# Performance work log

Measured on AMD Instinct MI355X. Metric: run time of the kernel, lower is better.

## Reference

```python
import jax, jax.numpy as jnp
import numpy as np
from jax import lax

EPS = 1e-5
KS = 3
PAD = 1
C = 256
G = 8          # ska_groups
VG = 8         # verifier groups
B, H, W = 8, 128, 128


def _bn(y, gamma, beta, mean, var):
    # inference-mode BatchNorm2d
    inv = gamma / jnp.sqrt(var + EPS)
    return y * inv[None, :, None, None] + (beta - mean * inv)[None, :, None, None]


def setup_inputs() -> dict:
    key = jax.random.key(0)
    ks = jax.random.split(key, 12)
    x = jax.random.normal(ks[0], (B, C, H, W), jnp.float32)
    dynamic_weight = jax.random.normal(ks[1], (B, G, KS * KS, H, W), jnp.float32)
    roi_mask = jax.random.uniform(ks[2], (B, 1, H, W), jnp.float32)
    # local_verifier params: Conv2d_BN(C,C,ks=3,pad=1,groups=8) -> ReLU -> Conv2d_BN(C,C,ks=1)
    w1 = jax.random.normal(ks[3], (C, C // VG, 3, 3), jnp.float32) * 0.05
    g1 = jnp.ones((C,), jnp.float32)
    b1 = jnp.zeros((C,), jnp.float32)
    m1 = jax.random.normal(ks[4], (C,), jnp.float32) * 0.1
    v1 = jax.random.uniform(ks[5], (C,), jnp.float32) + 0.5
    w2 = jax.random.normal(ks[6], (C, C, 1, 1), jnp.float32) * 0.05
    g2 = jnp.ones((C,), jnp.float32)
    b2 = jnp.zeros((C,), jnp.float32)
    m2 = jax.random.normal(ks[7], (C,), jnp.float32) * 0.1
    v2 = jax.random.uniform(ks[8], (C,), jnp.float32) + 0.5
    return dict(x=x, dynamic_weight=dynamic_weight, roi_mask=roi_mask,
                w1=w1, g1=g1, b1=b1, m1=m1, v1=v1,
                w2=w2, g2=g2, b2=b2, m2=m2, v2=v2)


def reference(x, dynamic_weight, roi_mask, w1, g1, b1, m1, v1, w2, g2, b2, m2, v2):
    Bx, Cx, Hx, Wx = x.shape
    gc = Cx // G  # group_channels
    # SKA: spatially-varying 3x3 aggregation. Boundary-dependent slicing in the
    # original is equivalent to zero-padding x by PAD.
    x_pad = jnp.pad(x, ((0, 0), (0, 0), (PAD, PAD), (PAD, PAD)))
    xg = x_pad.reshape(Bx, G, gc, Hx + 2 * PAD, Wx + 2 * PAD)
    ska = jnp.zeros((Bx, G, gc, Hx, Wx), x.dtype)
    for kh in range(KS):
        for kw in range(KS):
            ska = ska + xg[:, :, :, kh:kh + Hx, kw:kw + Wx] * \
                  dynamic_weight[:, :, None, kh * KS + kw]
    ska = ska.reshape(Bx, Cx, Hx, Wx)
    # local verifier: grouped 3x3 conv + BN + ReLU + 1x1 conv + BN
    y = ska * roi_mask
    y = lax.conv_general_dilated(y, w1, (1, 1), 'SAME',
                                 feature_group_count=VG,
                                 dimension_numbers=('NCHW', 'OIHW', 'NCHW'))
    y = jax.nn.relu(_bn(y, g1, b1, m1, v1))
    y = lax.conv_general_dilated(y, w2, (1, 1), 'VALID',
                                 dimension_numbers=('NCHW', 'OIHW', 'NCHW'))
    y = _bn(y, g2, b2, m2, v2)
    return ska + y
```

## Files before the change

### kernel.cpp

```cpp
#include <hip/hip_runtime.h>
#include <hip/hip_bf16.h>


#define HW 16384
#define EPS 1e-5f

typedef __bf16 bf16x8 __attribute__((ext_vector_type(8)));
typedef short short8 __attribute__((ext_vector_type(8)));
typedef short short4v __attribute__((ext_vector_type(4)));
typedef float floatx4 __attribute__((ext_vector_type(4)));

__device__ __forceinline__ unsigned short f2bf(float f) {
  unsigned u = __builtin_bit_cast(unsigned, f);
  unsigned r = u + 0x7FFFu + ((u >> 16) & 1u);
  return (unsigned short)(r >> 16);
}

__device__ __forceinline__ floatx4 mfma16(short8 a, short8 b, floatx4 c) {
  return __builtin_amdgcn_mfma_f32_16x16x32_bf16(
      __builtin_bit_cast(bf16x8, a), __builtin_bit_cast(bf16x8, b), c, 0, 0, 0);
}

__global__ __launch_bounds__(256) void prepack(const float* __restrict__ w1,
                                               const float* __restrict__ w2,
                                               unsigned short* __restrict__ w1b,
                                               unsigned short* __restrict__ w2b) {
  int o = blockIdx.x * 256 + threadIdx.x;
  if (o < 73728) {
    int ci  = o & 31;
    int co  = (o >> 5) & 31;
    int khw = (o >> 10) % 9;
    int g   = (o >> 10) / 9;
    w1b[o] = f2bf(w1[((g * 32 + co) * 32 + ci) * 9 + khw]);
  } else {
    int p = o - 73728;
    w2b[p] = f2bf(w2[p]);
  }
}

__global__ __launch_bounds__(256, 4) void ska_kernel(
    const float* __restrict__ x, const float* __restrict__ dw,
    const float* __restrict__ roi, float* __restrict__ out,
    unsigned short* __restrict__ y0b) {
  __shared__ float dwf[9][2][32];
  __shared__ float roib[2][32];
  __shared__ unsigned short tile[2 * 32 * 36];

  int phys = blockIdx.x;
  int blk  = (phys & 7) * 2048 + (phys >> 3);
  int wt = blk & 3;
  int hp = (blk >> 2) & 63;
  int g  = (blk >> 8) & 7;
  int b  = blk >> 11;
  int h0 = hp * 2;
  int tid = threadIdx.x;
  int ci = tid >> 3;
  int wq = tid & 7;
  int w0 = wt * 32 + wq * 4;
  int c  = g * 32 + ci;

  if (tid < 160) {
    if (tid < 144) {
      int k = tid >> 4, r = (tid >> 3) & 1, w4 = (tid & 7) * 4;
      *(floatx4*)&dwf[k][r][w4] = *(const floatx4*)
          &dw[((size_t)(b * 8 + g) * 9 + k) * HW + (h0 + r) * 128 + wt * 32 + w4];
    } else {
      int i = tid - 144, r = i >> 3, w4 = (i & 7) * 4;
      *(floatx4*)&roib[r][w4] = *(const floatx4*)
          &roi[(size_t)b * HW + (h0 + r) * 128 + wt * 32 + w4];
    }
  }

  float xr[4][6];
#pragma unroll
  for (int rr = 0; rr < 4; ++rr) {
    int hh = h0 - 1 + rr;
    if ((unsigned)hh < 128u) {
      const float* xp = &x[((size_t)(b * 256 + c)) * HW + hh * 128 + w0];
      floatx4 m = *(const floatx4*)xp;
      xr[rr][0] = (w0 > 0) ? xp[-1] : 0.f;
      xr[rr][1] = m[0];
      xr[rr][2] = m[1];
      xr[rr][3] = m[2];
      xr[rr][4] = m[3];
      xr[rr][5] = (w0 < 124) ? xp[4] : 0.f;
    } else {
#pragma unroll
      for (int i = 0; i < 6; ++i) xr[rr][i] = 0.f;
    }
  }

  __syncthreads();

  size_t base = ((size_t)(b * 256 + c)) * HW + h0 * 128 + w0;
#pragma unroll
  for (int r = 0; r < 2; ++r) {
    float s[4] = {0.f, 0.f, 0.f, 0.f};
#pragma unroll
    for (int kh = 0; kh < 3; ++kh)
#pragma unroll
      for (int kw = 0; kw < 3; ++kw) {
        floatx4 wk = *(const floatx4*)&dwf[kh * 3 + kw][r][wq * 4];
#pragma unroll
        for (int j = 0; j < 4; ++j) s[j] += xr[r + kh][kw + j] * wk[j];
      }
    *(floatx4*)&out[base + r * 128] = (floatx4){s[0], s[1], s[2], s[3]};
    floatx4 rv = *(const floatx4*)&roib[r][wq * 4];
#pragma unroll
    for (int j = 0; j < 4; ++j)
      tile[(r * 32 + wq * 4 + j) * 36 + ci] = f2bf(s[j] * rv[j]);
  }

  __syncthreads();

  unsigned short* dst =
      y0b + ((size_t)(b * 8 + g) * HW + h0 * 128 + wt * 32) * 32;
  int row = tid >> 7, rest = tid & 127;
  int w = rest >> 2, kk = rest & 3;
  *(short8*)&dst[(size_t)row * 128 * 32 + w * 32 + kk * 8] =
      *(const short8*)&tile[(row * 32 + w) * 36 + kk * 8];
}

__global__ __launch_bounds__(256) void conv1_mfma(
    const unsigned short* __restrict__ y0, const unsigned short* __restrict__ w1b,
    const float* __restrict__ g1, const float* __restrict__ b1,
    const float* __restrict__ m1, const float* __restrict__ v1,
    unsigned short* __restrict__ h1t) {
  __shared__ unsigned short xt[324 * 40];

  int blk  = blockIdx.x;
  int tile = blk & 63;
  int g    = (blk >> 6) & 7;
  int b    = blk >> 9;
  int h0   = (tile >> 3) * 16;
  int w0   = (tile & 7) * 16;
  int tid  = threadIdx.x;

  const unsigned short* xsrc = y0 + (size_t)(b * 8 + g) * HW * 32;
  short8 sv[6];
#pragma unroll
  for (int t = 0; t < 6; ++t) {
    int j = tid + t * 256;
    short8 v = (short8){0, 0, 0, 0, 0, 0, 0, 0};
    if (j < 1296) {
      int r = j >> 2, part = j & 3;
      int yy = r / 18, xx = r - yy * 18;
      int gh = h0 - 1 + yy, gw = w0 - 1 + xx;
      if ((unsigned)gh < 128u && (unsigned)gw < 128u)
        v = *(const short8*)&xsrc[(size_t)(gh * 128 + gw) * 32 + part * 8];
    }
    sv[t] = v;
  }
#pragma unroll
  for (int t = 0; t < 6; ++t) {
    int j = tid + t * 256;
    if (j < 1296) {
      int r = j >> 2, part = j & 3;
      *(short8*)&xt[r * 40 + part * 8] = sv[t];
    }
  }

  int wv = tid >> 6, lane = tid & 63, q = lane >> 4, n = lane & 15;

  short8 bf[9][2];
  const unsigned short* wgb = w1b + (size_t)g * 9 * 32 * 32;
#pragma unroll
  for (int khw = 0; khw < 9; ++khw) {
#pragma unroll
    for (int half = 0; half < 2; ++half)
      bf[khw][half] =
          *(const short8*)&wgb[(khw * 32 + half * 16 + n) * 32 + q * 8];
  }

  __syncthreads();

  floatx4 acc[4][2];
#pragma unroll
  for (int r = 0; r < 4; ++r)
#pragma unroll
    for (int half = 0; half < 2; ++half) acc[r][half] = (floatx4){0.f, 0.f, 0.f, 0.f};

#pragma unroll
  for (int r = 0; r < 4; ++r) {
    int row = wv * 4 + r;
#pragma unroll
    for (int khw = 0; khw < 9; ++khw) {
      int kh = khw / 3, kw = khw % 3;
      short8 a = *(const short8*)&xt[((row + kh) * 18 + kw + n) * 40 + q * 8];
      acc[r][0] = mfma16(a, bf[khw][0], acc[r][0]);
      acc[r][1] = mfma16(a, bf[khw][1], acc[r][1]);
    }
  }

  float inv[2], bias[2];
#pragma unroll
  for (int half = 0; half < 2; ++half) {
    int cc = g * 32 + half * 16 + n;
    inv[half]  = g1[cc] * rsqrtf(v1[cc] + EPS);
    bias[half] = b1[cc] - m1[cc] * inv[half];
  }

  __syncthreads();

#pragma unroll
  for (int r = 0; r < 4; ++r) {
    int pr = (wv * 4 + r) * 16;
#pragma unroll
    for (int half = 0; half < 2; ++half) {
      int co = half * 16 + n;
#pragma unroll
      for (int reg = 0; reg < 4; ++reg) {
        int px = pr + q * 4 + reg;
        float v = fmaxf(acc[r][half][reg] * inv[half] + bias[half], 0.f);
        xt[px * 40 + co] = f2bf(v);
      }
    }
  }

  __syncthreads();

  unsigned short* hb = h1t + (size_t)(b * 8 + g) * HW * 32;
  int ph = tid >> 4, pw = tid & 15;
  size_t gp = (size_t)((h0 + ph) * 128 + (w0 + pw)) * 32;
#pragma unroll
  for (int k = 0; k < 4; ++k)
    *(short8*)&hb[gp + k * 8] = *(const short8*)&xt[tid * 40 + k * 8];
}

__global__ __launch_bounds__(256) void conv2_mfma(
    const unsigned short* __restrict__ h1t, const unsigned short* __restrict__ w2b,
    const float* __restrict__ g2, const float* __restrict__ b2,
    const float* __restrict__ m2, const float* __restrict__ v2,
    float* __restrict__ out) {
  __shared__ unsigned short As[3][2048];

  int blk = blockIdx.x;
  int b   = blk >> 8;
  int px0 = (blk & 255) * 64;
  int tid = threadIdx.x;
  int wv = tid >> 6, lane = tid & 63, q = lane >> 4, n = lane & 15;

  const unsigned short* sb = h1t + ((size_t)b * 8 * HW + px0) * 32;

#define STAGE(S, BUF)                                                         \
  __builtin_amdgcn_global_load_lds(                                           \
      (const __attribute__((address_space(1))) unsigned int*)(sb +            \
          (size_t)(S) * HW * 32 + wv * 512 + lane * 8),                       \
      (__attribute__((address_space(3))) unsigned int*)&As[BUF][wv * 512],    \
      16, 0, 0)

  floatx4 acc[4][4];
#pragma unroll
  for (int mt = 0; mt < 4; ++mt)
#pragma unroll
    for (int nt = 0; nt < 4; ++nt) acc[mt][nt] = (floatx4){0.f, 0.f, 0.f, 0.f};

  STAGE(0, 0);
  STAGE(1, 1);
  asm volatile("s_waitcnt vmcnt(1)");
  __syncthreads();

#pragma unroll
  for (int s = 0; s < 8; ++s) {
    if (s < 6) STAGE(s + 2, (s + 2) % 3);
    short8 bb[4];
#pragma unroll
    for (int nt = 0; nt < 4; ++nt)
      bb[nt] =
          *(const short8*)&w2b[(wv * 64 + nt * 16 + n) * 256 + s * 32 + q * 8];
    const unsigned short* Ab = &As[s % 3][0];
#pragma unroll
    for (int mt = 0; mt < 4; ++mt) {
      short8 a = *(const short8*)&Ab[(mt * 16 + n) * 32 + q * 8];
#pragma unroll
      for (int nt = 0; nt < 4; ++nt) acc[mt][nt] = mfma16(a, bb[nt], acc[mt][nt]);
    }
    if (s < 6) asm volatile("s_waitcnt vmcnt(1)");
    else if (s == 6) asm volatile("s_waitcnt vmcnt(0)");
    if (s < 7) __syncthreads();
  }
#undef STAGE

#pragma unroll
  for (int nt = 0; nt < 4; ++nt) {
    int co = wv * 64 + nt * 16 + n;
    float inv  = g2[co] * rsqrtf(v2[co] + EPS);
    float bias = b2[co] - m2[co] * inv;
    float* ob = out + (size_t)(b * 256 + co) * HW;
#pragma unroll
    for (int mt = 0; mt < 4; ++mt) {
      int px = px0 + mt * 16 + q * 4;
      float4 sv = *(float4*)&ob[px];
      sv.x += acc[mt][nt][0] * inv + bias;
      sv.y += acc[mt][nt][1] * inv + bias;
      sv.z += acc[mt][nt][2] * inv + bias;
      sv.w += acc[mt][nt][3] * inv + bias;
      *(float4*)&ob[px] = sv;
    }
  }
}

extern "C" void kernel_launch(void* const* d_in, const int* in_sizes, int n_in,
                              void* d_out, int out_size, void* d_ws,
                              size_t ws_size, hipStream_t stream) {
  const float* x   = (const float*)d_in[0];
  const float* dw  = (const float*)d_in[1];
  const float* roi = (const float*)d_in[2];
  const float* w1  = (const float*)d_in[3];
  const float* g1  = (const float*)d_in[4];
  const float* b1  = (const float*)d_in[5];
  const float* m1  = (const float*)d_in[6];
  const float* v1  = (const float*)d_in[7];
  const float* w2  = (const float*)d_in[8];
  const float* g2  = (const float*)d_in[9];
  const float* b2  = (const float*)d_in[10];
  const float* m2  = (const float*)d_in[11];
  const float* v2  = (const float*)d_in[12];
  float* out = (float*)d_out;

  char* ws = (char*)d_ws;
  unsigned short* y0b = (unsigned short*)ws;
  unsigned short* h1t = (unsigned short*)(ws + 67108864);
  unsigned short* w1b = (unsigned short*)(ws + 134217728);
  unsigned short* w2b = (unsigned short*)(ws + 134365184);

  prepack<<<544, 256, 0, stream>>>(w1, w2, w1b, w2b);
  ska_kernel<<<16384, 256, 0, stream>>>(x, dw, roi, out, y0b);
  conv1_mfma<<<4096, 256, 0, stream>>>(y0b, w1b, g1, b1, m1, v1, h1t);
  conv2_mfma<<<2048, 256, 0, stream>>>(h1t, w2b, g2, b2, m2, v2, out);
}
```

Measured before the change: 459.8 us.

## Fold weight prepack into SKA kernel and process one row per block

Removes the separate prepack launch by appending extra blocks to the SKA kernel that convert w1/w2 to bf16. Each SKA block now handles a single output row instead of two, loading the dynamic weights and ROI mask straight into registers instead of staging them in shared memory. This doubles the grid size and re-reads the halo rows of x more often, in exchange for dropping one kernel launch and one barrier. The tile padding and store width change to match the single-row layout.

```diff
diff --git a/kernel.cpp b/kernel.cpp
--- a/kernel.cpp
+++ b/kernel.cpp
@@ -21,104 +21,91 @@
       __builtin_bit_cast(bf16x8, a), __builtin_bit_cast(bf16x8, b), c, 0, 0, 0);
 }
 
-__global__ __launch_bounds__(256) void prepack(const float* __restrict__ w1,
-                                               const float* __restrict__ w2,
-                                               unsigned short* __restrict__ w1b,
-                                               unsigned short* __restrict__ w2b) {
-  int o = blockIdx.x * 256 + threadIdx.x;
-  if (o < 73728) {
-    int ci  = o & 31;
-    int co  = (o >> 5) & 31;
-    int khw = (o >> 10) % 9;
-    int g   = (o >> 10) / 9;
-    w1b[o] = f2bf(w1[((g * 32 + co) * 32 + ci) * 9 + khw]);
-  } else {
-    int p = o - 73728;
-    w2b[p] = f2bf(w2[p]);
-  }
-}
-
 __global__ __launch_bounds__(256, 4) void ska_kernel(
     const float* __restrict__ x, const float* __restrict__ dw,
     const float* __restrict__ roi, float* __restrict__ out,
-    unsigned short* __restrict__ y0b) {
-  __shared__ float dwf[9][2][32];
-  __shared__ float roib[2][32];
-  __shared__ unsigned short tile[2 * 32 * 36];
+    unsigned short* __restrict__ y0b,
+    const float* __restrict__ w1, const float* __restrict__ w2,
+    unsigned short* __restrict__ w1b, unsigned short* __restrict__ w2b) {
+  __shared__ unsigned short tile[32 * 34];
 
   int phys = blockIdx.x;
-  int blk  = (phys & 7) * 2048 + (phys >> 3);
+  int tid  = threadIdx.x;
+
+  if (phys >= 32768) {
+    int o = (phys - 32768) * 256 + tid;
+    if (o < 73728) {
+      int ci  = o & 31;
+      int co  = (o >> 5) & 31;
+      int khw = (o >> 10) % 9;
+      int g   = (o >> 10) / 9;
+      w1b[o] = f2bf(w1[((g * 32 + co) * 32 + ci) * 9 + khw]);
+    } else {
+      int p = o - 73728;
+      w2b[p] = f2bf(w2[p]);
+    }
+    return;
+  }
+
+  int blk = (phys & 7) * 4096 + (phys >> 3);
   int wt = blk & 3;
-  int hp = (blk >> 2) & 63;
-  int g  = (blk >> 8) & 7;
-  int b  = blk >> 11;
-  int h0 = hp * 2;
-  int tid = threadIdx.x;
+  int h  = (blk >> 2) & 127;
+  int g  = (blk >> 9) & 7;
+  int b  = blk >> 12;
   int ci = tid >> 3;
   int wq = tid & 7;
   int w0 = wt * 32 + wq * 4;
   int c  = g * 32 + ci;
 
-  if (tid < 160) {
-    if (tid < 144) {
-      int k = tid >> 4, r = (tid >> 3) & 1, w4 = (tid & 7) * 4;
-      *(floatx4*)&dwf[k][r][w4] = *(const floatx4*)
-          &dw[((size_t)(b * 8 + g) * 9 + k) * HW + (h0 + r) * 128 + wt * 32 + w4];
+  const float* dwb = dw + ((size_t)(b * 8 + g) * 9) * HW + h * 128 + w0;
+  floatx4 wv[9];
+#pragma unroll
+  for (int k = 0; k < 9; ++k) wv[k] = *(const floatx4*)&dwb[k * HW];
+
+  floatx4 rv = *(const floatx4*)&roi[(size_t)b * HW + h * 128 + w0];
+
+  size_t base = ((size_t)(b * 256 + c)) * HW + h * 128 + w0;
+  float xr[3][6];
+#pragma unroll
+  for (int kh = 0; kh < 3; ++kh) {
+    int hh = h + kh - 1;
+    if ((unsigned)hh < 128u) {
+      const float* xp = &x[base + (kh - 1) * 128];
+      floatx4 m = *(const floatx4*)xp;
+      xr[kh][0] = (w0 > 0) ? xp[-1] : 0.f;
+      xr[kh][1] = m[0];
+      xr[kh][2] = m[1];
+      xr[kh][3] = m[2];
+      xr[kh][4] = m[3];
+      xr[kh][5] = (w0 < 124) ? xp[4] : 0.f;
     } else {
-      int i = tid - 144, r = i >> 3, w4 = (i & 7) * 4;
-      *(floatx4*)&roib[r][w4] = *(const floatx4*)
-          &roi[(size_t)b * HW + (h0 + r) * 128 + wt * 32 + w4];
-    }
-  }
-
-  float xr[4][6];
-#pragma unroll
-  for (int rr = 0; rr < 4; ++rr) {
-    int hh = h0 - 1 + rr;
-    if ((unsigned)hh < 128u) {
-      const float* xp = &x[((size_t)(b * 256 + c)) * HW + hh * 128 + w0];
-      floatx4 m = *(const floatx4*)xp;
-      xr[rr][0] = (w0 > 0) ? xp[-1] : 0.f;
-      xr[rr][1] = m[0];
-      xr[rr][2] = m[1];
-      xr[rr][3] = m[2];
-      xr[rr][4] = m[3];
-      xr[rr][5] = (w0 < 124) ? xp[4] : 0.f;
-    } else {
-#pragma unroll
-      for (int i = 0; i < 6; ++i) xr[rr][i] = 0.f;
-    }
-  }
-
-  __syncthreads();
-
-  size_t base = ((size_t)(b * 256 + c)) * HW + h0 * 128 + w0;
-#pragma unroll
-  for (int r = 0; r < 2; ++r) {
-    float s[4] = {0.f, 0.f, 0.f, 0.f};
-#pragma unroll
-    for (int kh = 0; kh < 3; ++kh)
-#pragma unroll
-      for (int kw = 0; kw < 3; ++kw) {
-        floatx4 wk = *(const floatx4*)&dwf[kh * 3 + kw][r][wq * 4];
-#pragma unroll
-        for (int j = 0; j < 4; ++j) s[j] += xr[r + kh][kw + j] * wk[j];
-      }
-    *(floatx4*)&out[base + r * 128] = (floatx4){s[0], s[1], s[2], s[3]};
-    floatx4 rv = *(const floatx4*)&roib[r][wq * 4];
-#pragma unroll
-    for (int j = 0; j < 4; ++j)
-      tile[(r * 32 + wq * 4 + j) * 36 + ci] = f2bf(s[j] * rv[j]);
-  }
+#pragma unroll
+      for (int i = 0; i < 6; ++i) xr[kh][i] = 0.f;
+    }
+  }
+
+  float s[4] = {0.f, 0.f, 0.f, 0.f};
+#pragma unroll
+  for (int kh = 0; kh < 3; ++kh)
+#pragma unroll
+    for (int kw = 0; kw < 3; ++kw) {
+      floatx4 wk = wv[kh * 3 + kw];
+#pragma unroll
+      for (int j = 0; j < 4; ++j) s[j] += xr[kh][kw + j] * wk[j];
+    }
+
+  *(floatx4*)&out[base] = (floatx4){s[0], s[1], s[2], s[3]};
+
+#pragma unroll
+  for (int j = 0; j < 4; ++j)
+    tile[(wq * 4 + j) * 34 + ci] = f2bf(s[j] * rv[j]);
 
   __syncthreads();
 
   unsigned short* dst =
-      y0b + ((size_t)(b * 8 + g) * HW + h0 * 128 + wt * 32) * 32;
-  int row = tid >> 7, rest = tid & 127;
-  int w = rest >> 2, kk = rest & 3;
-  *(short8*)&dst[(size_t)row * 128 * 32 + w * 32 + kk * 8] =
-      *(const short8*)&tile[(row * 32 + w) * 36 + kk * 8];
+      y0b + ((size_t)(b * 8 + g) * HW + h * 128 + wt * 32) * 32;
+  int w = tid >> 3, k = tid & 7;
+  *(short4v*)&dst[tid * 4] = *(const short4v*)&tile[w * 34 + k * 4];
 }
 
 __global__ __launch_bounds__(256) void conv1_mfma(
@@ -324,8 +311,7 @@
   unsigned short* w1b = (unsigned short*)(ws + 134217728);
   unsigned short* w2b = (unsigned short*)(ws + 134365184);
 
-  prepack<<<544, 256, 0, stream>>>(w1, w2, w1b, w2b);
-  ska_kernel<<<16384, 256, 0, stream>>>(x, dw, roi, out, y0b);
+  ska_kernel<<<33312, 256, 0, stream>>>(x, dw, roi, out, y0b, w1, w2, w1b, w2b);
   conv1_mfma<<<4096, 256, 0, stream>>>(y0b, w1b, g1, b1, m1, v1, h1t);
   conv2_mfma<<<2048, 256, 0, stream>>>(h1t, w2b, g2, b2, m2, v2, out);
 }
```

After: 512.0 us. 11.3% more time.
